# Optimization experiments

Measured on AMD Instinct MI355X. Metric: run time of the kernel, lower is better.

Reference implementation:

```python
import jax, jax.numpy as jnp
import numpy as np

B = 4096
NP = 196  # 14*14 patches
NW = 4    # qubits


def setup_inputs() -> dict:
    key = jax.random.key(0)
    ks = jax.random.split(key, 6)
    x = jax.random.normal(ks[0], (B, 1, 28, 28), dtype=jnp.float32)
    conv_w = jax.random.normal(ks[1], (4, 1, 2, 2), dtype=jnp.float32) * 0.5
    conv_b = jax.random.normal(ks[2], (4,), dtype=jnp.float32) * 0.1
    q_theta = jax.random.uniform(ks[3], (4,), dtype=jnp.float32, minval=0.0, maxval=2.0 * np.pi)
    lin_w = jax.random.normal(ks[4], (10, 784), dtype=jnp.float32) * 0.03
    lin_b = jnp.zeros((10,), dtype=jnp.float32)
    return {"x": x, "conv_w": conv_w, "conv_b": conv_b, "q_theta": q_theta,
            "lin_w": lin_w, "lin_b": lin_b}


def _apply_1q(state, U, wire):
    # state: [N,2,2,2,2] complex, wire axis = wire+1
    s = jnp.moveaxis(state, wire + 1, -1)
    s = jnp.einsum('...a,ba->...b', s, U)
    return jnp.moveaxis(s, -1, wire + 1)


def _apply_cnot(state, ctrl, tgt):
    s = jnp.moveaxis(state, (ctrl + 1, tgt + 1), (-2, -1))  # [...,c,t]
    s = jnp.stack([s[..., 0, :], s[..., 1, ::-1]], axis=-2)
    return jnp.moveaxis(s, (-2, -1), (ctrl + 1, tgt + 1))


def _ry(t):
    c, s = jnp.cos(t), jnp.sin(t)
    return jnp.stack([jnp.stack([c, -s]), jnp.stack([s, c])]).astype(jnp.complex64)


def _rx(t):
    c, s = jnp.cos(t).astype(jnp.complex64), jnp.sin(t).astype(jnp.complex64)
    return jnp.stack([jnp.stack([c, -1j * s]), jnp.stack([-1j * s, c])])


def _rz(t):
    e = jnp.exp(-1j * t.astype(jnp.complex64))
    z = jnp.zeros((), jnp.complex64)
    return jnp.stack([jnp.stack([e, z]), jnp.stack([z, jnp.conj(e)])])


def _quantum_features(angles, q_theta):
    # angles: [N,4] encoding Ry angles; starts from |0000> per patch (encoder resets state)
    h = 0.5 * angles
    q = jnp.stack([jnp.cos(h), jnp.sin(h)], axis=-1).astype(jnp.complex64)  # [N,4,2]
    state = jnp.einsum('na,nb,nc,nd->nabcd', q[:, 0], q[:, 1], q[:, 2], q[:, 3])
    th = 0.5 * q_theta
    # fixed 8-op random layer: 4 rotations + 4 CNOTs
    state = _apply_1q(state, _ry(th[0]), 0)
    state = _apply_1q(state, _rx(th[1]), 1)
    state = _apply_1q(state, _rz(th[2]), 2)
    state = _apply_1q(state, _ry(th[3]), 3)
    state = _apply_cnot(state, 0, 1)
    state = _apply_cnot(state, 1, 2)
    state = _apply_cnot(state, 2, 3)
    state = _apply_cnot(state, 0, 3)
    probs = state.real ** 2 + state.imag ** 2  # [N,2,2,2,2]
    ez = []
    for w in range(NW):
        axes = tuple(a for a in range(1, 5) if a != w + 1)
        p = probs.sum(axis=axes)  # [N,2]
        ez.append(p[:, 0] - p[:, 1])
    return jnp.stack(ez, axis=-1)  # [N,4] <Z_w> expectations


def reference(x, conv_w, conv_b, q_theta, lin_w, lin_b):
    feats = jax.lax.conv_general_dilated(
        x, conv_w, window_strides=(2, 2), padding='VALID',
        dimension_numbers=('NCHW', 'OIHW', 'NCHW')) + conv_b[None, :, None, None]
    bsz = feats.shape[0]
    flat = feats.reshape(bsz, -1)                    # [B, 4*14*14] channel-major
    patches = flat.reshape(bsz, 14, 14, 4)           # as in torch .view
    angles = patches.reshape(bsz * NP, NW)           # patch-major over (r,c)
    qf = _quantum_features(angles, q_theta).reshape(bsz, NP * NW).astype(jnp.float32)
    logits = qf @ lin_w.T + lin_b
    return jax.nn.log_softmax(logits, axis=-1)
```

## Files before the change

### kernel.cpp

```cpp
#include <hip/hip_runtime.h>
#include <math.h>


#define NB 4096

__global__ __launch_bounds__(256) void hqe_kernel(
    const float* __restrict__ x,
    const float* __restrict__ conv_w,
    const float* __restrict__ conv_b,
    const float* __restrict__ q_theta,
    const float* __restrict__ lin_w,
    const float* __restrict__ lin_b,
    float* __restrict__ out)
{
    __shared__ __align__(16) float xs[784];
    __shared__ __align__(16) float qf[784];
    __shared__ float logits_s[10];

    const int b = blockIdx.x;
    const int t = threadIdx.x;
    const int wave = t >> 6;
    const int lane = t & 63;

    if (t < 196) {
        ((float4*)xs)[t] = ((const float4*)(x + b * 784))[t];
    } else if (t < 206) {
        logits_s[t - 196] = lin_b[t - 196];
    }

    const float th0 = q_theta[0];
    const float ct1 = __cosf(q_theta[1]);
    const float th3 = q_theta[3];

    __syncthreads();

    if (t < 196) {
        const int c = t / 49;
        const int rbase = 4 * t - 196 * c;
        const float4 cw = ((const float4*)conv_w)[c];
        const float cb = conv_b[c];
        float a[4];
#pragma unroll
        for (int k = 0; k < 4; ++k) {
            const int s = rbase + k;
            const int h = s / 14;
            const int w = s - 14 * h;
            const float* xp = xs + 56 * h + 2 * w;
            a[k] = cb + xp[0] * cw.x + xp[1] * cw.y + xp[28] * cw.z + xp[29] * cw.w;
        }
        const float z0 = __cosf(a[0] + th0);
        const float z1 = ct1 * __cosf(a[1]);
        const float z2 = __cosf(a[2]);
        const float z3 = __cosf(a[3] + th3);
        const float f1 = z0 * z1;
        const float f2 = f1 * z2;
        const float f3 = z1 * z2 * z3;
        ((float4*)qf)[t] = make_float4(z0, f1, f2, f3);
    }

    __syncthreads();

    const float4* q4 = (const float4*)qf;
    const float4 q0 = q4[lane];
    const float4 q1 = q4[64 + lane];
    const float4 q2 = q4[128 + lane];
    float4 q3 = make_float4(0.f, 0.f, 0.f, 0.f);
    if (lane < 4) q3 = q4[192 + lane];

    for (int o = wave; o < 10; o += 4) {
        const float4* wv = (const float4*)(lin_w + o * 784);
        const float4 w0 = wv[lane];
        const float4 w1 = wv[64 + lane];
        const float4 w2 = wv[128 + lane];
        float s = q0.x * w0.x + q0.y * w0.y + q0.z * w0.z + q0.w * w0.w;
        s += q1.x * w1.x + q1.y * w1.y + q1.z * w1.z + q1.w * w1.w;
        s += q2.x * w2.x + q2.y * w2.y + q2.z * w2.z + q2.w * w2.w;
        if (lane < 4) {
            const float4 w3 = wv[192 + lane];
            s += q3.x * w3.x + q3.y * w3.y + q3.z * w3.z + q3.w * w3.w;
        }
#pragma unroll
        for (int off = 32; off > 0; off >>= 1)
            s += __shfl_down(s, off, 64);
        if (lane == 0) logits_s[o] += s;
    }

    __syncthreads();

    if (t < 10) {
        float m = -INFINITY;
#pragma unroll
        for (int j = 0; j < 10; ++j) m = fmaxf(m, logits_s[j]);
        float sum = 0.0f;
#pragma unroll
        for (int j = 0; j < 10; ++j) sum += __expf(logits_s[j] - m);
        out[b * 10 + t] = logits_s[t] - m - __logf(sum);
    }
}

extern "C" void kernel_launch(void* const* d_in, const int* in_sizes, int n_in,
                              void* d_out, int out_size, void* d_ws, size_t ws_size,
                              hipStream_t stream) {
    const float* x       = (const float*)d_in[0];
    const float* conv_w  = (const float*)d_in[1];
    const float* conv_b  = (const float*)d_in[2];
    const float* q_theta = (const float*)d_in[3];
    const float* lin_w   = (const float*)d_in[4];
    const float* lin_b   = (const float*)d_in[5];
    float* out = (float*)d_out;

    hqe_kernel<<<dim3(NB), dim3(256), 0, stream>>>(x, conv_w, conv_b, q_theta,
                                                   lin_w, lin_b, out);
}
```

Before: 78.41 us.

## Process eight images per block and keep linear weights in registers

```diff
diff --git a/kernel.cpp b/kernel.cpp
--- a/kernel.cpp
+++ b/kernel.cpp
@@ -2,7 +2,9 @@
 #include <math.h>
 
 
-#define NB 4096
+#define NB    4096
+#define BPB   8
+#define GRID  (NB / BPB)
 
 __global__ __launch_bounds__(256) void hqe_kernel(
     const float* __restrict__ x,
@@ -13,39 +15,59 @@
     const float* __restrict__ lin_b,
     float* __restrict__ out)
 {
-    __shared__ __align__(16) float xs[784];
-    __shared__ __align__(16) float qf[784];
-    __shared__ float logits_s[10];
+    __shared__ __align__(16) float xs[BPB * 784];
+    __shared__ __align__(16) float qf[BPB * 784];
+    __shared__ float logits_s[BPB][10];
 
-    const int b = blockIdx.x;
     const int t = threadIdx.x;
     const int wave = t >> 6;
     const int lane = t & 63;
+    const int b0 = blockIdx.x * BPB;
 
-    if (t < 196) {
-        ((float4*)xs)[t] = ((const float4*)(x + b * 784))[t];
-    } else if (t < 206) {
-        logits_s[t - 196] = lin_b[t - 196];
+    {
+        const float4* src = (const float4*)(x + (size_t)b0 * 784);
+        float4* dst = (float4*)xs;
+        for (int i = t; i < BPB * 196; i += 256) dst[i] = src[i];
     }
+    if (t < BPB * 10) logits_s[t / 10][t % 10] = lin_b[t % 10];
 
     const float th0 = q_theta[0];
     const float ct1 = __cosf(q_theta[1]);
     const float th3 = q_theta[3];
 
+    float4 wreg[3][4];
+    int nout = 0;
+#pragma unroll
+    for (int oi = 0; oi < 3; ++oi) {
+        const int o = wave + 4 * oi;
+        if (o < 10) {
+            const float4* wv = (const float4*)(lin_w + o * 784);
+            wreg[oi][0] = wv[lane];
+            wreg[oi][1] = wv[64 + lane];
+            wreg[oi][2] = wv[128 + lane];
+            wreg[oi][3] = (lane < 4) ? wv[192 + lane]
+                                     : make_float4(0.f, 0.f, 0.f, 0.f);
+            nout = oi + 1;
+        }
+    }
+
     __syncthreads();
 
-    if (t < 196) {
-        const int c = t / 49;
-        const int rbase = 4 * t - 196 * c;
+    for (int i = t; i < BPB * 196; i += 256) {
+        const int bb = i / 196;
+        const int p = i - 196 * bb;
+        const int c = p / 49;
+        const int rbase = 4 * p - 196 * c;
         const float4 cw = ((const float4*)conv_w)[c];
         const float cb = conv_b[c];
+        const float* xb = xs + bb * 784;
         float a[4];
 #pragma unroll
         for (int k = 0; k < 4; ++k) {
             const int s = rbase + k;
             const int h = s / 14;
             const int w = s - 14 * h;
-            const float* xp = xs + 56 * h + 2 * w;
+            const float* xp = xb + 56 * h + 2 * w;
             a[k] = cb + xp[0] * cw.x + xp[1] * cw.y + xp[28] * cw.z + xp[29] * cw.w;
         }
         const float z0 = __cosf(a[0] + th0);
@@ -55,46 +77,47 @@
         const float f1 = z0 * z1;
         const float f2 = f1 * z2;
         const float f3 = z1 * z2 * z3;
-        ((float4*)qf)[t] = make_float4(z0, f1, f2, f3);
+        ((float4*)qf)[i] = make_float4(z0, f1, f2, f3);
     }
 
     __syncthreads();
 
-    const float4* q4 = (const float4*)qf;
-    const float4 q0 = q4[lane];
-    const float4 q1 = q4[64 + lane];
-    const float4 q2 = q4[128 + lane];
-    float4 q3 = make_float4(0.f, 0.f, 0.f, 0.f);
-    if (lane < 4) q3 = q4[192 + lane];
-
-    for (int o = wave; o < 10; o += 4) {
-        const float4* wv = (const float4*)(lin_w + o * 784);
-        const float4 w0 = wv[lane];
-        const float4 w1 = wv[64 + lane];
-        const float4 w2 = wv[128 + lane];
-        float s = q0.x * w0.x + q0.y * w0.y + q0.z * w0.z + q0.w * w0.w;
-        s += q1.x * w1.x + q1.y * w1.y + q1.z * w1.z + q1.w * w1.w;
-        s += q2.x * w2.x + q2.y * w2.y + q2.z * w2.z + q2.w * w2.w;
-        if (lane < 4) {
-            const float4 w3 = wv[192 + lane];
-            s += q3.x * w3.x + q3.y * w3.y + q3.z * w3.z + q3.w * w3.w;
+    for (int bb = 0; bb < BPB; ++bb) {
+        const float4* q4 = (const float4*)(qf + bb * 784);
+        const float4 q0 = q4[lane];
+        const float4 q1 = q4[64 + lane];
+        const float4 q2 = q4[128 + lane];
+        const float4 q3 = (lane < 4) ? q4[192 + lane]
+                                     : make_float4(0.f, 0.f, 0.f, 0.f);
+        for (int oi = 0; oi < nout; ++oi) {
+            float s;
+            s  = q0.x * wreg[oi][0].x + q0.y * wreg[oi][0].y
+               + q0.z * wreg[oi][0].z + q0.w * wreg[oi][0].w;
+            s += q1.x * wreg[oi][1].x + q1.y * wreg[oi][1].y
+               + q1.z * wreg[oi][1].z + q1.w * wreg[oi][1].w;
+            s += q2.x * wreg[oi][2].x + q2.y * wreg[oi][2].y
+               + q2.z * wreg[oi][2].z + q2.w * wreg[oi][2].w;
+            s += q3.x * wreg[oi][3].x + q3.y * wreg[oi][3].y
+               + q3.z * wreg[oi][3].z + q3.w * wreg[oi][3].w;
+#pragma unroll
+            for (int off = 32; off > 0; off >>= 1)
+                s += __shfl_down(s, off, 64);
+            if (lane == 0) logits_s[bb][wave + 4 * oi] += s;
         }
-#pragma unroll
-        for (int off = 32; off > 0; off >>= 1)
-            s += __shfl_down(s, off, 64);
-        if (lane == 0) logits_s[o] += s;
     }
 
     __syncthreads();
 
-    if (t < 10) {
+    if (t < BPB * 10) {
+        const int bb = t / 10;
+        const int j = t - 10 * bb;
         float m = -INFINITY;
 #pragma unroll
-        for (int j = 0; j < 10; ++j) m = fmaxf(m, logits_s[j]);
+        for (int k = 0; k < 10; ++k) m = fmaxf(m, logits_s[bb][k]);
         float sum = 0.0f;
 #pragma unroll
-        for (int j = 0; j < 10; ++j) sum += __expf(logits_s[j] - m);
-        out[b * 10 + t] = logits_s[t] - m - __logf(sum);
+        for (int k = 0; k < 10; ++k) sum += __expf(logits_s[bb][k] - m);
+        out[(size_t)(b0 + bb) * 10 + j] = logits_s[bb][j] - m - __logf(sum);
     }
 }
 
@@ -109,6 +132,6 @@
     const float* lin_b   = (const float*)d_in[5];
     float* out = (float*)d_out;
 
-    hqe_kernel<<<dim3(NB), dim3(256), 0, stream>>>(x, conv_w, conv_b, q_theta,
-                                                   lin_w, lin_b, out);
+    hqe_kernel<<<dim3(GRID), dim3(256), 0, stream>>>(x, conv_w, conv_b, q_theta,
+                                                     lin_w, lin_b, out);
 }
```

After: 97.53 us. 1.24x slower.

## Batch 8 samples per block and compute linear layer with bf16 MFMA

Applied to the files above, without the earlier changes.

```diff
diff --git a/kernel.cpp b/kernel.cpp
--- a/kernel.cpp
+++ b/kernel.cpp
@@ -2,7 +2,19 @@
 #include <math.h>
 
 
-#define NB 4096
+#define NB   4096
+#define BPB  8
+#define GRID (NB / BPB)
+#define KP   896
+#define RS   904
+
+using short8  = __attribute__((ext_vector_type(8))) short;
+using float4v = __attribute__((ext_vector_type(4))) float;
+
+__device__ __forceinline__ unsigned short f2bf(float f) {
+    unsigned u = __builtin_bit_cast(unsigned, f);
+    return (unsigned short)((u + 0x7FFFu + ((u >> 16) & 1u)) >> 16);
+}
 
 __global__ __launch_bounds__(256) void hqe_kernel(
     const float* __restrict__ x,
@@ -13,40 +25,59 @@
     const float* __restrict__ lin_b,
     float* __restrict__ out)
 {
-    __shared__ __align__(16) float xs[784];
-    __shared__ __align__(16) float qf[784];
-    __shared__ float logits_s[10];
+    __shared__ __align__(16) unsigned short qf_s[16 * RS];
+    __shared__ __align__(16) unsigned short w_s[16 * RS];
+    __shared__ __align__(16) float red_s[4 * 16 * 16];
+    __shared__ float lg_s[BPB * 10];
+    __shared__ float off_s[BPB];
 
-    const int b = blockIdx.x;
     const int t = threadIdx.x;
-    const int wave = t >> 6;
-    const int lane = t & 63;
+    const int b0 = blockIdx.x * BPB;
 
-    if (t < 196) {
-        ((float4*)xs)[t] = ((const float4*)(x + b * 784))[t];
-    } else if (t < 206) {
-        logits_s[t - 196] = lin_b[t - 196];
+    for (int i = t; i < 8 * 56; i += 256) {
+        const int r = i / 56, d = i - 56 * r;
+        ((unsigned*)(qf_s + r * RS + 784))[d] = 0u;
+    }
+    for (int i = t; i < 10 * 56; i += 256) {
+        const int r = i / 56, d = i - 56 * r;
+        ((unsigned*)(w_s + r * RS + 784))[d] = 0u;
+    }
+
+    {
+        const float4* lw4 = (const float4*)lin_w;
+        for (int i = t; i < 1960; i += 256) {
+            const int o = i / 196;
+            const int k0 = 4 * (i - 196 * o);
+            const float4 v = lw4[i];
+            const unsigned lo = f2bf(v.x) | ((unsigned)f2bf(v.y) << 16);
+            const unsigned hi = f2bf(v.z) | ((unsigned)f2bf(v.w) << 16);
+            *(uint2*)(w_s + o * RS + k0) = make_uint2(lo, hi);
+        }
     }
 
     const float th0 = q_theta[0];
     const float ct1 = __cosf(q_theta[1]);
     const float th3 = q_theta[3];
 
-    __syncthreads();
-
-    if (t < 196) {
-        const int c = t / 49;
-        const int rbase = 4 * t - 196 * c;
+    for (int i = t; i < BPB * 196; i += 256) {
+        const int b = i / 196;
+        const int p = i - 196 * b;
+        const int c = p / 49;
+        const int s0 = 4 * p - 196 * c;
         const float4 cw = ((const float4*)conv_w)[c];
         const float cb = conv_b[c];
+        const float* xb = x + (size_t)(b0 + b) * 784;
+
         float a[4];
 #pragma unroll
-        for (int k = 0; k < 4; ++k) {
-            const int s = rbase + k;
+        for (int j = 0; j < 4; ++j) {
+            const int s = s0 + j;
             const int h = s / 14;
-            const int w = s - 14 * h;
-            const float* xp = xs + 56 * h + 2 * w;
-            a[k] = cb + xp[0] * cw.x + xp[1] * cw.y + xp[28] * cw.z + xp[29] * cw.w;
+            const int w2 = s - 14 * h;
+            const float* xp = xb + h * 56 + 2 * w2;
+            const float2 top = *(const float2*)xp;
+            const float2 bot = *(const float2*)(xp + 28);
+            a[j] = cb + top.x * cw.x + top.y * cw.y + bot.x * cw.z + bot.y * cw.w;
         }
         const float z0 = __cosf(a[0] + th0);
         const float z1 = ct1 * __cosf(a[1]);
@@ -55,46 +86,60 @@
         const float f1 = z0 * z1;
         const float f2 = f1 * z2;
         const float f3 = z1 * z2 * z3;
-        ((float4*)qf)[t] = make_float4(z0, f1, f2, f3);
+        const unsigned lo = f2bf(z0) | ((unsigned)f2bf(f1) << 16);
+        const unsigned hi = f2bf(f2) | ((unsigned)f2bf(f3) << 16);
+        *(uint2*)(qf_s + b * RS + 4 * p) = make_uint2(lo, hi);
     }
 
     __syncthreads();
 
-    const float4* q4 = (const float4*)qf;
-    const float4 q0 = q4[lane];
-    const float4 q1 = q4[64 + lane];
-    const float4 q2 = q4[128 + lane];
-    float4 q3 = make_float4(0.f, 0.f, 0.f, 0.f);
-    if (lane < 4) q3 = q4[192 + lane];
-
-    for (int o = wave; o < 10; o += 4) {
-        const float4* wv = (const float4*)(lin_w + o * 784);
-        const float4 w0 = wv[lane];
-        const float4 w1 = wv[64 + lane];
-        const float4 w2 = wv[128 + lane];
-        float s = q0.x * w0.x + q0.y * w0.y + q0.z * w0.z + q0.w * w0.w;
-        s += q1.x * w1.x + q1.y * w1.y + q1.z * w1.z + q1.w * w1.w;
-        s += q2.x * w2.x + q2.y * w2.y + q2.z * w2.z + q2.w * w2.w;
-        if (lane < 4) {
-            const float4 w3 = wv[192 + lane];
-            s += q3.x * w3.x + q3.y * w3.y + q3.z * w3.z + q3.w * w3.w;
+    {
+        const int wv = t >> 6;
+        const int lane = t & 63;
+        const int mrow = lane & 15;
+        const int qd = lane >> 4;
+        const unsigned short* qrow = qf_s + mrow * RS;
+        const unsigned short* wrow = w_s + mrow * RS;
+        float4v acc = {0.f, 0.f, 0.f, 0.f};
+        const int kbase = 224 * wv + 8 * qd;
+#pragma unroll
+        for (int kk = 0; kk < 7; ++kk) {
+            const int k = kbase + 32 * kk;
+            const short8 af = *(const short8*)(qrow + k);
+            const short8 bf = *(const short8*)(wrow + k);
+            acc = __builtin_amdgcn_mfma_f32_16x16x32_bf16(af, bf, acc, 0, 0, 0);
         }
-#pragma unroll
-        for (int off = 32; off > 0; off >>= 1)
-            s += __shfl_down(s, off, 64);
-        if (lane == 0) logits_s[o] += s;
+        *(float4v*)(red_s + (wv * 16 + mrow) * 16 + qd * 4) = acc;
     }
 
     __syncthreads();
 
-    if (t < 10) {
-        float m = -INFINITY;
+    {
+        const int n = t >> 4;
+        const int m = t & 15;
+        if (m < BPB && n < 10) {
+            const float s = red_s[0 * 256 + n * 16 + m] + red_s[1 * 256 + n * 16 + m]
+                          + red_s[2 * 256 + n * 16 + m] + red_s[3 * 256 + n * 16 + m];
+            lg_s[m * 10 + n] = s + lin_b[n];
+        }
+    }
+
+    __syncthreads();
+
+    if (t < BPB) {
+        float mx = -INFINITY;
 #pragma unroll
-        for (int j = 0; j < 10; ++j) m = fmaxf(m, logits_s[j]);
+        for (int j = 0; j < 10; ++j) mx = fmaxf(mx, lg_s[t * 10 + j]);
         float sum = 0.0f;
 #pragma unroll
-        for (int j = 0; j < 10; ++j) sum += __expf(logits_s[j] - m);
-        out[b * 10 + t] = logits_s[t] - m - __logf(sum);
+        for (int j = 0; j < 10; ++j) sum += __expf(lg_s[t * 10 + j] - mx);
+        off_s[t] = mx + __logf(sum);
+    }
+
+    __syncthreads();
+
+    if (t < BPB * 10) {
+        out[(size_t)b0 * 10 + t] = lg_s[t] - off_s[t / 10];
     }
 }
 
@@ -109,6 +154,6 @@
     const float* lin_b   = (const float*)d_in[5];
     float* out = (float*)d_out;
 
-    hqe_kernel<<<dim3(NB), dim3(256), 0, stream>>>(x, conv_w, conv_b, q_theta,
-                                                   lin_w, lin_b, out);
+    hqe_kernel<<<dim3(GRID), dim3(256), 0, stream>>>(x, conv_w, conv_b, q_theta,
+                                                     lin_w, lin_b, out);
 }
```

Result: faster. 74.87 us (-4.5%).
